# Kernel tuning notes

Hardware: AMD Instinct MI355X
Metric: run time of the kernel (lower is better)

## Reference

```python
import jax, jax.numpy as jnp
import numpy as np
import math

B, T, C = 1, 4096, 2048
N_HEAD, N_KV = 16, 4
HD = C // N_HEAD            # 128
QPK = N_HEAD // N_KV        # 4
WINDOW = 1024
QKV_OUT = (N_HEAD + 2 * N_KV) * HD  # 3072


def setup_inputs() -> dict:
    key = jax.random.key(0)
    k1, k2, k3 = jax.random.split(key, 3)
    x = jax.random.normal(k1, (B, T, C), dtype=jnp.float32)
    W_attn = jax.random.normal(k2, (C, QKV_OUT), dtype=jnp.float32) * 0.02
    W_proj = jax.random.normal(k3, (C, C), dtype=jnp.float32) * 0.02
    # RoPE table: (T, HD//2, 2) = (cos, sin)
    inv_freq = 1.0 / (10000.0 ** (np.arange(0, HD, 2, dtype=np.float32) / HD))
    t = np.arange(T, dtype=np.float32)
    ang = np.outer(t, inv_freq)  # (T, HD//2)
    freqs_cis = jnp.asarray(np.stack([np.cos(ang), np.sin(ang)], axis=-1))
    return {"x": x, "freqs_cis": freqs_cis, "W_attn": W_attn, "W_proj": W_proj}


def apply_rope(xh, freqs_cis):
    # xh: (B, T, H, D); freqs_cis: (T, D//2, 2)
    b, t, h, d = xh.shape
    xs = xh.astype(jnp.float32).reshape(b, t, h, d // 2, 2)
    fc = freqs_cis.reshape(1, t, 1, d // 2, 2)
    re = xs[..., 0] * fc[..., 0] - xs[..., 1] * fc[..., 1]
    im = xs[..., 1] * fc[..., 0] + xs[..., 0] * fc[..., 1]
    return jnp.stack([re, im], axis=-1).reshape(b, t, h, d).astype(xh.dtype)


def reference(x, freqs_cis, W_attn, W_proj):
    qkv = x @ W_attn                                    # (B, T, 3072)
    tot = QPK + 2
    qkv = qkv.reshape(B, T, N_KV, tot, HD)
    qkv = jnp.transpose(qkv, (0, 2, 3, 1, 4))           # (B, n_kv, tot, T, hd)
    q = qkv[:, :, :QPK]                                 # (B, n_kv, qpk, T, hd)
    k = qkv[:, :, QPK:QPK + 1]
    v = qkv[:, :, QPK + 1:]
    # Faithful to torch: raw contiguous reshape (scrambles head/time layout)
    q = q.reshape(B, -1, N_HEAD, HD)                    # (B, T, n_head, hd)
    k = k.reshape(B, -1, N_KV, HD)
    v = v.reshape(B, -1, N_KV, HD)
    q = apply_rope(q, freqs_cis)
    k = apply_rope(k, freqs_cis)
    # GQA: physical repeat_interleave of K/V heads
    k = jnp.repeat(k, QPK, axis=2)                      # (B, T, n_head, hd)
    v = jnp.repeat(v, QPK, axis=2)
    q = jnp.transpose(q, (0, 2, 1, 3))                  # (B, n_head, T, hd)
    k = jnp.transpose(k, (0, 2, 1, 3))
    v = jnp.transpose(v, (0, 2, 1, 3))
    scores = jnp.einsum("bhqd,bhkd->bhqk", q, k) / math.sqrt(HD)
    # Symmetric band mask (triu(-w+1) * tril(w-1)): |i-j| <= w-1. NOT causal.
    i = jnp.arange(T)[:, None]
    j = jnp.arange(T)[None, :]
    band = jnp.abs(i - j) <= (WINDOW - 1)               # (T, T) bool
    scores = jnp.where(band[None, None], scores, -jnp.inf)
    probs = jax.nn.softmax(scores.astype(jnp.float32), axis=-1).astype(q.dtype)
    y = jnp.einsum("bhqk,bhkd->bhqd", probs, v)         # (B, n_head, T, hd)
    y = jnp.transpose(y, (0, 2, 1, 3)).reshape(B, T, C)
    return y @ W_proj
```

## Files before the change

### kernel.cpp

```cpp
#include <hip/hip_runtime.h>
#include <hip/hip_bf16.h>

typedef __attribute__((ext_vector_type(8))) short short8;
typedef __attribute__((ext_vector_type(4))) float f32x4;

static constexpr int Tt   = 4096;
static constexpr int Cc   = 2048;
static constexpr int NH   = 16;
static constexpr int HD   = 128;
static constexpr int QKVO = 3072;
static constexpr int W1   = 1023;

#define GLDS16(gp, lp)                                                        \
  __builtin_amdgcn_global_load_lds(                                           \
      (const __attribute__((address_space(1))) unsigned int*)(gp),            \
      (__attribute__((address_space(3))) unsigned int*)(lp), 16, 0, 0)

__global__ void cvt4(const float* __restrict__ in,
                     __hip_bfloat16* __restrict__ out, int n) {
  int i = (blockIdx.x * blockDim.x + threadIdx.x) * 4;
  if (i >= n) return;
  float4 v = *(const float4*)&in[i];
  union { ushort4 u; __hip_bfloat16 b[4]; } o;
  o.b[0] = __float2bfloat16(v.x);
  o.b[1] = __float2bfloat16(v.y);
  o.b[2] = __float2bfloat16(v.z);
  o.b[3] = __float2bfloat16(v.w);
  *(ushort4*)&out[i] = o.u;
}

__global__ void tconv(const float* __restrict__ W,
                      __hip_bfloat16* __restrict__ Wt, int K, int N) {
  __shared__ float tile[32][33];
  const int k0 = blockIdx.x * 32, n0 = blockIdx.y * 32;
  const int tx = threadIdx.x, ty = threadIdx.y;
#pragma unroll
  for (int r = 0; r < 4; ++r)
    tile[ty * 4 + r][tx] = W[(size_t)(k0 + ty * 4 + r) * N + n0 + tx];
  __syncthreads();
#pragma unroll
  for (int r = 0; r < 4; ++r)
    Wt[(size_t)(n0 + ty * 4 + r) * K + k0 + tx] =
        __float2bfloat16(tile[tx][ty * 4 + r]);
}

__global__ void vtrans(const __hip_bfloat16* __restrict__ vb,
                       __hip_bfloat16* __restrict__ vbt) {
  __shared__ unsigned short tile[32][34];
  const int t0 = blockIdx.x * 32, d0 = blockIdx.y * 32, kvh = blockIdx.z;
  const int tx = threadIdx.x, ty = threadIdx.y;
#pragma unroll
  for (int r = 0; r < 4; ++r)
    tile[ty * 4 + r][tx] =
        *(const unsigned short*)&vb[(size_t)(t0 + ty * 4 + r) * 512 +
                                    kvh * HD + d0 + tx];
  __syncthreads();
#pragma unroll
  for (int r = 0; r < 4; ++r)
    *(unsigned short*)&vbt[(size_t)kvh * 524288 + (size_t)(d0 + ty * 4 + r) * Tt +
                           t0 + tx] = tile[tx][ty * 4 + r];
}

template <bool OUT_BF16>
__global__ __launch_bounds__(256) void gemm_bt(
    const __hip_bfloat16* __restrict__ A, const __hip_bfloat16* __restrict__ Bt,
    void* __restrict__ Cout, int M, int N, int K) {
  __shared__ __hip_bfloat16 As[128 * 32];
  __shared__ __hip_bfloat16 Bs[128 * 32];
  const int tid = threadIdx.x;
  const int lane = tid & 63, wid = tid >> 6;
  const int l15 = lane & 15, lhi = lane >> 4;
  const int m0 = blockIdx.y * 128, n0 = blockIdx.x * 128;
  const int wm = wid >> 1, wn = wid & 1;
  f32x4 acc[4][4] = {};
  for (int k0 = 0; k0 < K; k0 += 32) {
#pragma unroll
    for (int cc = 0; cc < 2; ++cc) {
      const int ebase = cc * 2048 + wid * 512;
      const int el = ebase + lane * 8;
      const int row = el >> 5, col = el & 31;
      GLDS16(A + (size_t)(m0 + row) * K + k0 + col, As + ebase);
      GLDS16(Bt + (size_t)(n0 + row) * K + k0 + col, Bs + ebase);
    }
    __syncthreads();
    short8 af[4], bfr[4];
#pragma unroll
    for (int i = 0; i < 4; ++i)
      af[i] = *(const short8*)&As[(wm * 64 + i * 16 + l15) * 32 + lhi * 8];
#pragma unroll
    for (int j = 0; j < 4; ++j)
      bfr[j] = *(const short8*)&Bs[(wn * 64 + j * 16 + l15) * 32 + lhi * 8];
#pragma unroll
    for (int i = 0; i < 4; ++i)
#pragma unroll
      for (int j = 0; j < 4; ++j)
        acc[i][j] = __builtin_amdgcn_mfma_f32_16x16x32_bf16(af[i], bfr[j],
                                                            acc[i][j], 0, 0, 0);
    __syncthreads();
  }
#pragma unroll
  for (int i = 0; i < 4; ++i)
#pragma unroll
    for (int r = 0; r < 4; ++r) {
      const int row = m0 + wm * 64 + i * 16 + lhi * 4 + r;
#pragma unroll
      for (int j = 0; j < 4; ++j) {
        const int col = n0 + wn * 64 + j * 16 + l15;
        if (OUT_BF16)
          ((__hip_bfloat16*)Cout)[(size_t)row * N + col] =
              __float2bfloat16(acc[i][j][r]);
        else
          ((float*)Cout)[(size_t)row * N + col] = acc[i][j][r];
      }
    }
}

__global__ void rope_scatter(const __hip_bfloat16* __restrict__ qkv,
                             const float* __restrict__ fc,
                             __hip_bfloat16* __restrict__ qb,
                             __hip_bfloat16* __restrict__ kb,
                             __hip_bfloat16* __restrict__ vb) {
  const int p = blockIdx.x * blockDim.x + threadIdx.x;
  const int t = blockIdx.y;
  const int c = p * 2;
  const int kv = c / 768;
  const int rem = c - kv * 768;
  const int slot = rem >> 7;
  const int d = rem & 127;
  const ushort2 xy = *(const ushort2*)&qkv[(size_t)t * QKVO + c];
  const float x0 = __bfloat162float(*(const __hip_bfloat16*)&xy.x);
  const float x1 = __bfloat162float(*(const __hip_bfloat16*)&xy.y);
  union { ushort2 uu; __hip_bfloat16 b[2]; } o;
  if (slot < 4) {
    const unsigned u = ((unsigned)kv << 14) | ((unsigned)slot << 12) | (unsigned)t;
    const int tp = u >> 4, h = u & 15;
    const float2 cs = *(const float2*)&fc[(size_t)tp * 128 + (d >> 1) * 2];
    o.b[0] = __float2bfloat16(x0 * cs.x - x1 * cs.y);
    o.b[1] = __float2bfloat16(x1 * cs.x + x0 * cs.y);
    *(ushort2*)&qb[(size_t)tp * Cc + h * HD + d] = o.uu;
  } else {
    const unsigned u2 = ((unsigned)kv << 12) | (unsigned)t;
    const int tp = u2 >> 2, hk = u2 & 3;
    if (slot == 4) {
      const float2 cs = *(const float2*)&fc[(size_t)tp * 128 + (d >> 1) * 2];
      o.b[0] = __float2bfloat16(x0 * cs.x - x1 * cs.y);
      o.b[1] = __float2bfloat16(x1 * cs.x + x0 * cs.y);
      *(ushort2*)&kb[(size_t)tp * 512 + hk * HD + d] = o.uu;
    } else {
      o.uu = xy;
      *(ushort2*)&vb[(size_t)tp * 512 + hk * HD + d] = o.uu;
    }
  }
}

__global__ __launch_bounds__(512) void attn_band(
    const __hip_bfloat16* __restrict__ qb, const __hip_bfloat16* __restrict__ kb,
    const __hip_bfloat16* __restrict__ vbt, __hip_bfloat16* __restrict__ yb) {
  __shared__ __hip_bfloat16 kt[2][64 * 128];
  __shared__ __hip_bfloat16 vt[2][128 * 64];
  __shared__ __hip_bfloat16 pl[8][16 * 64];
  const int tid = threadIdx.x, lane = tid & 63, wid = tid >> 6;
  const int l15 = lane & 15, lhi = lane >> 4;
  const int q0 = blockIdx.x * 128, h = blockIdx.y;
  const int kvh = h >> 2;
  const int qrow = q0 + wid * 16 + l15;
  short8 aq[4];
#pragma unroll
  for (int kc = 0; kc < 4; ++kc)
    aq[kc] = *(const short8*)&qb[(size_t)qrow * Cc + h * HD + kc * 32 + lhi * 8];
  f32x4 o[8] = {};
  float mrow[4] = {-1e30f, -1e30f, -1e30f, -1e30f};
  float lrow[4] = {0.f, 0.f, 0.f, 0.f};
  const int js = (q0 - W1 > 0 ? q0 - W1 : 0) & ~63;
  const int jeu = q0 + 128 + W1;
  const int je = jeu < Tt ? jeu : Tt;
  const int nt = (je - js + 63) >> 6;
  const float scale = 0.08838834764831845f;
  char* ktb = (char*)kt;
  char* vtb = (char*)vt;
  char* plc = (char*)&pl[wid][0];
  const size_t vbase = (size_t)kvh * 524288;

  auto stage = [&](int j0, int buf) {
    char* kd = ktb + buf * 16384;
    char* vd = vtb + buf * 16384;
#pragma unroll
    for (int cc = 0; cc < 2; ++cc) {
      const int sb = (cc * 8 + wid) << 10;
      {
        const int S = sb + lane * 16;
        const int row = S >> 8;
        const int colb = (S & 255) ^ ((row & 7) << 4);
        int jc = j0 + row;
        jc = jc < Tt - 1 ? jc : Tt - 1;
        GLDS16(kb + (size_t)jc * 512 + kvh * HD + (colb >> 1), kd + sb);
      }
      {
        const int S = sb + lane * 16;
        const int row = S >> 7;
        const int colb = (S & 127) ^ ((row & 7) << 4);
        GLDS16(vbt + vbase + (size_t)row * Tt + j0 + (colb >> 1), vd + sb);
      }
    }
  };

  stage(js, 0);
  int cur = 0;
  for (int t = 0; t < nt; ++t) {
    const int j0 = js + t * 64;
    __syncthreads();
    if (t + 1 < nt) stage(j0 + 64, cur ^ 1);
    char* ktc = ktb + cur * 16384;
    char* vtc = vtb + cur * 16384;
    f32x4 s[4] = {};
#pragma unroll
    for (int jt = 0; jt < 4; ++jt) {
      const int row = jt * 16 + l15;
      const int sw = (row & 7) << 4;
#pragma unroll
      for (int kc = 0; kc < 4; ++kc) {
        const short8 bk =
            *(const short8*)(ktc + row * 256 + ((kc * 64 + lhi * 16) ^ sw));
        s[jt] = __builtin_amdgcn_mfma_f32_16x16x32_bf16(aq[kc], bk, s[jt], 0, 0, 0);
      }
    }
    float val[4][4], pm[4];
#pragma unroll
    for (int jt = 0; jt < 4; ++jt)
#pragma unroll
      for (int r = 0; r < 4; ++r) {
        const int j = j0 + jt * 16 + l15;
        const int i = q0 + wid * 16 + lhi * 4 + r;
        const int diff = i > j ? i - j : j - i;
        const bool ok = (j < Tt) && (diff <= W1);
        val[jt][r] = ok ? s[jt][r] * scale : -1e30f;
      }
#pragma unroll
    for (int r = 0; r < 4; ++r) {
      float v = fmaxf(fmaxf(val[0][r], val[1][r]), fmaxf(val[2][r], val[3][r]));
      v = fmaxf(v, __shfl_xor(v, 1));
      v = fmaxf(v, __shfl_xor(v, 2));
      v = fmaxf(v, __shfl_xor(v, 4));
      v = fmaxf(v, __shfl_xor(v, 8));
      pm[r] = v;
    }
    float need = 0.f;
#pragma unroll
    for (int r = 0; r < 4; ++r) need = fmaxf(need, pm[r] - mrow[r]);
    if (!__all(need <= 8.0f)) {
#pragma unroll
      for (int r = 0; r < 4; ++r) {
        const float mn = fmaxf(mrow[r], pm[r]);
        const float esc = __expf(mrow[r] - mn);
        mrow[r] = mn;
        lrow[r] *= esc;
#pragma unroll
        for (int dt = 0; dt < 8; ++dt) o[dt][r] *= esc;
      }
    }
    float rs[4] = {0.f, 0.f, 0.f, 0.f};
#pragma unroll
    for (int jt = 0; jt < 4; ++jt)
#pragma unroll
      for (int r = 0; r < 4; ++r) {
        const float p = __expf(val[jt][r] - mrow[r]);
        rs[r] += p;
        const int row = lhi * 4 + r;
        const int b = row * 128 + (((jt * 16 + l15) * 2) ^ ((row & 7) << 4));
        *(__hip_bfloat16*)(plc + b) = __float2bfloat16(p);
      }
#pragma unroll
    for (int r = 0; r < 4; ++r) {
      float v = rs[r];
      v += __shfl_xor(v, 1);
      v += __shfl_xor(v, 2);
      v += __shfl_xor(v, 4);
      v += __shfl_xor(v, 8);
      lrow[r] += v;
    }
    const int psw = (l15 & 7) << 4;
    const short8 pa0 = *(const short8*)(plc + l15 * 128 + ((lhi * 16) ^ psw));
    const short8 pa1 = *(const short8*)(plc + l15 * 128 + ((64 + lhi * 16) ^ psw));
#pragma unroll
    for (int dt = 0; dt < 8; ++dt) {
      const int d = dt * 16 + l15;
      const int vsw = (d & 7) << 4;
      const short8 bv0 = *(const short8*)(vtc + d * 128 + ((lhi * 16) ^ vsw));
      const short8 bv1 = *(const short8*)(vtc + d * 128 + ((64 + lhi * 16) ^ vsw));
      o[dt] = __builtin_amdgcn_mfma_f32_16x16x32_bf16(pa0, bv0, o[dt], 0, 0, 0);
      o[dt] = __builtin_amdgcn_mfma_f32_16x16x32_bf16(pa1, bv1, o[dt], 0, 0, 0);
    }
    cur ^= 1;
  }
#pragma unroll
  for (int dt = 0; dt < 8; ++dt)
#pragma unroll
    for (int r = 0; r < 4; ++r) {
      const int i = q0 + wid * 16 + lhi * 4 + r;
      yb[(size_t)i * Cc + h * HD + dt * 16 + l15] =
          __float2bfloat16(o[dt][r] / lrow[r]);
    }
}

extern "C" void kernel_launch(void* const* d_in, const int* in_sizes, int n_in,
                              void* d_out, int out_size, void* d_ws,
                              size_t ws_size, hipStream_t stream) {
  const float* x = (const float*)d_in[0];
  const float* fc = (const float*)d_in[1];
  const float* Wa = (const float*)d_in[2];
  const float* Wp = (const float*)d_in[3];
  float* out = (float*)d_out;
  char* ws = (char*)d_ws;
  __hip_bfloat16* xb  = (__hip_bfloat16*)(ws);
  __hip_bfloat16* Wat = (__hip_bfloat16*)(ws + (16u << 20));
  __hip_bfloat16* Wpt = (__hip_bfloat16*)(ws + (28u << 20));
  __hip_bfloat16* qkv = (__hip_bfloat16*)(ws + (36u << 20));
  __hip_bfloat16* qb  = (__hip_bfloat16*)(ws);
  __hip_bfloat16* kb  = (__hip_bfloat16*)(ws + (16u << 20));
  __hip_bfloat16* vb  = (__hip_bfloat16*)(ws + (20u << 20));
  __hip_bfloat16* vbt = (__hip_bfloat16*)(ws + (24u << 20));
  __hip_bfloat16* yb  = qkv;

  cvt4<<<dim3(Tt * Cc / 1024), 256, 0, stream>>>(x, xb, Tt * Cc);
  tconv<<<dim3(Cc / 32, QKVO / 32), dim3(32, 8), 0, stream>>>(Wa, Wat, Cc, QKVO);
  tconv<<<dim3(Cc / 32, Cc / 32), dim3(32, 8), 0, stream>>>(Wp, Wpt, Cc, Cc);
  gemm_bt<true><<<dim3(QKVO / 128, Tt / 128), 256, 0, stream>>>(
      xb, Wat, qkv, Tt, QKVO, Cc);
  rope_scatter<<<dim3(6, Tt), 256, 0, stream>>>(qkv, fc, qb, kb, vb);
  vtrans<<<dim3(Tt / 32, HD / 32, 4), dim3(32, 8), 0, stream>>>(vb, vbt);
  attn_band<<<dim3(Tt / 128, NH), 512, 0, stream>>>(qb, kb, vbt, yb);
  gemm_bt<false><<<dim3(Cc / 128, Tt / 128), 256, 0, stream>>>(
      yb, Wpt, out, Tt, Cc, Cc);
}
```

Baseline: 460.0 us.

## Single-buffer V tiles, defer row-sum reduction, and raise MFMA wave priority

The V tile is now single-buffered and loaded at the start of each iteration, overlapping with the QK^T MFMAs, while K stays double-buffered. This cuts LDS use, and a new __syncthreads is placed before the PV stage. The per-iteration cross-lane row-sum reduction becomes a per-lane partial sum that is rescaled alongside the output and reduced once after the loop. s_setprio brackets around both MFMA blocks try to favour matrix-issuing waves. The trade-off is an extra block barrier per tile and V load latency that is no longer prefetched a full iteration ahead.

```diff
diff --git a/kernel.cpp b/kernel.cpp
--- a/kernel.cpp
+++ b/kernel.cpp
@@ -157,7 +157,7 @@
     const __hip_bfloat16* __restrict__ qb, const __hip_bfloat16* __restrict__ kb,
     const __hip_bfloat16* __restrict__ vbt, __hip_bfloat16* __restrict__ yb) {
   __shared__ __hip_bfloat16 kt[2][64 * 128];
-  __shared__ __hip_bfloat16 vt[2][128 * 64];
+  __shared__ __hip_bfloat16 vt[128 * 64];
   __shared__ __hip_bfloat16 pl[8][16 * 64];
   const int tid = threadIdx.x, lane = tid & 63, wid = tid >> 6;
   const int l15 = lane & 15, lhi = lane >> 4;
@@ -170,49 +170,51 @@
     aq[kc] = *(const short8*)&qb[(size_t)qrow * Cc + h * HD + kc * 32 + lhi * 8];
   f32x4 o[8] = {};
   float mrow[4] = {-1e30f, -1e30f, -1e30f, -1e30f};
-  float lrow[4] = {0.f, 0.f, 0.f, 0.f};
+  float lsum[4] = {0.f, 0.f, 0.f, 0.f};
   const int js = (q0 - W1 > 0 ? q0 - W1 : 0) & ~63;
   const int jeu = q0 + 128 + W1;
   const int je = jeu < Tt ? jeu : Tt;
   const int nt = (je - js + 63) >> 6;
   const float scale = 0.08838834764831845f;
   char* ktb = (char*)kt;
-  char* vtb = (char*)vt;
+  char* vtc = (char*)vt;
   char* plc = (char*)&pl[wid][0];
   const size_t vbase = (size_t)kvh * 524288;
 
-  auto stage = [&](int j0, int buf) {
+  auto stageK = [&](int j0, int buf) {
     char* kd = ktb + buf * 16384;
-    char* vd = vtb + buf * 16384;
 #pragma unroll
     for (int cc = 0; cc < 2; ++cc) {
       const int sb = (cc * 8 + wid) << 10;
-      {
-        const int S = sb + lane * 16;
-        const int row = S >> 8;
-        const int colb = (S & 255) ^ ((row & 7) << 4);
-        int jc = j0 + row;
-        jc = jc < Tt - 1 ? jc : Tt - 1;
-        GLDS16(kb + (size_t)jc * 512 + kvh * HD + (colb >> 1), kd + sb);
-      }
-      {
-        const int S = sb + lane * 16;
-        const int row = S >> 7;
-        const int colb = (S & 127) ^ ((row & 7) << 4);
-        GLDS16(vbt + vbase + (size_t)row * Tt + j0 + (colb >> 1), vd + sb);
-      }
+      const int S = sb + lane * 16;
+      const int row = S >> 8;
+      const int colb = (S & 255) ^ ((row & 7) << 4);
+      int jc = j0 + row;
+      jc = jc < Tt - 1 ? jc : Tt - 1;
+      GLDS16(kb + (size_t)jc * 512 + kvh * HD + (colb >> 1), kd + sb);
     }
   };
-
-  stage(js, 0);
+  auto stageV = [&](int j0) {
+#pragma unroll
+    for (int cc = 0; cc < 2; ++cc) {
+      const int sb = (cc * 8 + wid) << 10;
+      const int S = sb + lane * 16;
+      const int row = S >> 7;
+      const int colb = (S & 127) ^ ((row & 7) << 4);
+      GLDS16(vbt + vbase + (size_t)row * Tt + j0 + (colb >> 1), vtc + sb);
+    }
+  };
+
+  stageK(js, 0);
   int cur = 0;
   for (int t = 0; t < nt; ++t) {
     const int j0 = js + t * 64;
     __syncthreads();
-    if (t + 1 < nt) stage(j0 + 64, cur ^ 1);
+    stageV(j0);
+    if (t + 1 < nt) stageK(j0 + 64, cur ^ 1);
     char* ktc = ktb + cur * 16384;
-    char* vtc = vtb + cur * 16384;
     f32x4 s[4] = {};
+    __builtin_amdgcn_s_setprio(1);
 #pragma unroll
     for (int jt = 0; jt < 4; ++jt) {
       const int row = jt * 16 + l15;
@@ -224,6 +226,7 @@
         s[jt] = __builtin_amdgcn_mfma_f32_16x16x32_bf16(aq[kc], bk, s[jt], 0, 0, 0);
       }
     }
+    __builtin_amdgcn_s_setprio(0);
     float val[4][4], pm[4];
 #pragma unroll
     for (int jt = 0; jt < 4; ++jt)
@@ -253,34 +256,26 @@
         const float mn = fmaxf(mrow[r], pm[r]);
         const float esc = __expf(mrow[r] - mn);
         mrow[r] = mn;
-        lrow[r] *= esc;
+        lsum[r] *= esc;
 #pragma unroll
         for (int dt = 0; dt < 8; ++dt) o[dt][r] *= esc;
       }
     }
-    float rs[4] = {0.f, 0.f, 0.f, 0.f};
 #pragma unroll
     for (int jt = 0; jt < 4; ++jt)
 #pragma unroll
       for (int r = 0; r < 4; ++r) {
         const float p = __expf(val[jt][r] - mrow[r]);
-        rs[r] += p;
+        lsum[r] += p;
         const int row = lhi * 4 + r;
         const int b = row * 128 + (((jt * 16 + l15) * 2) ^ ((row & 7) << 4));
         *(__hip_bfloat16*)(plc + b) = __float2bfloat16(p);
       }
-#pragma unroll
-    for (int r = 0; r < 4; ++r) {
-      float v = rs[r];
-      v += __shfl_xor(v, 1);
-      v += __shfl_xor(v, 2);
-      v += __shfl_xor(v, 4);
-      v += __shfl_xor(v, 8);
-      lrow[r] += v;
-    }
+    __syncthreads();
     const int psw = (l15 & 7) << 4;
     const short8 pa0 = *(const short8*)(plc + l15 * 128 + ((lhi * 16) ^ psw));
     const short8 pa1 = *(const short8*)(plc + l15 * 128 + ((64 + lhi * 16) ^ psw));
+    __builtin_amdgcn_s_setprio(1);
 #pragma unroll
     for (int dt = 0; dt < 8; ++dt) {
       const int d = dt * 16 + l15;
@@ -290,7 +285,18 @@
       o[dt] = __builtin_amdgcn_mfma_f32_16x16x32_bf16(pa0, bv0, o[dt], 0, 0, 0);
       o[dt] = __builtin_amdgcn_mfma_f32_16x16x32_bf16(pa1, bv1, o[dt], 0, 0, 0);
     }
+    __builtin_amdgcn_s_setprio(0);
     cur ^= 1;
+  }
+  float lrow[4];
+#pragma unroll
+  for (int r = 0; r < 4; ++r) {
+    float v = lsum[r];
+    v += __shfl_xor(v, 1);
+    v += __shfl_xor(v, 2);
+    v += __shfl_xor(v, 4);
+    v += __shfl_xor(v, 8);
+    lrow[r] = v;
   }
 #pragma unroll
   for (int dt = 0; dt < 8; ++dt)
```

New measurement: 415.0 us. -9.8%, faster.
